# Optimization experiments

Hardware: AMD Instinct MI355X
Metric: run time of the kernel (lower is better)

## Reference

```python
import jax, jax.numpy as jnp
import numpy as np

ROPE_BASE = 10000.0

def _rms_norm(x):
    eps = jnp.asarray(jnp.finfo(x.dtype).eps, x.dtype)
    return x * jax.lax.rsqrt(jnp.mean(x * x, axis=-1, keepdims=True) + eps)

def _rope(x):
    # x: [B, S, H, hd]; rotate-halves variant: y1 = x1*cos + x2*sin, y2 = -x1*sin + x2*cos
    S, hd = x.shape[1], x.shape[3]
    d = hd // 2
    inv_freq = 1.0 / (ROPE_BASE ** (jnp.arange(0, hd, 2, dtype=jnp.float32) / hd))  # [d]
    t = jnp.arange(S, dtype=jnp.float32)
    freqs = jnp.outer(t, inv_freq)                       # [S, d]
    cos = jnp.cos(freqs)[None, :, None, :].astype(x.dtype)
    sin = jnp.sin(freqs)[None, :, None, :].astype(x.dtype)
    x1, x2 = x[..., :d], x[..., d:]
    return jnp.concatenate([x1 * cos + x2 * sin, -x1 * sin + x2 * cos], axis=-1)

def setup_inputs() -> dict:
    key = jax.random.key(0)
    ks = jax.random.split(key, 7)
    B, S, D = 1, 2048, 1024
    std = 0.02
    return {
        "x": jax.random.normal(ks[0], (B, S, D), jnp.float32),
        "v1": jax.random.normal(ks[1], (B, S, D), jnp.float32),
        "Wq": jax.random.normal(ks[2], (D, D), jnp.float32) * std,
        "Wk": jax.random.normal(ks[3], (D, D), jnp.float32) * std,
        "Wv": jax.random.normal(ks[4], (D, D), jnp.float32) * std,
        "Wout": jax.random.normal(ks[5], (D, D), jnp.float32) * std,
        "lambdas": jnp.float32(0.5),
        "n_heads": 16,
    }

def reference(x, v1, Wq, Wk, Wv, Wout, lambdas, n_heads):
    B, S, D = x.shape
    H = n_heads
    hd = D // H
    # QKV projections (CastedLinear, no bias)
    q = (x @ Wq.T).reshape(B, S, H, hd)
    k = (x @ Wk.T).reshape(B, S, H, hd)
    v = (x @ Wv.T).reshape(B, S, H, hd)
    # value residual mix with first-layer values v1
    v = (1.0 - lambdas) * v + lambdas * v1.reshape(B, S, H, hd)
    # per-head RMS norm (no learned scale) then RoPE
    q, k = _rms_norm(q), _rms_norm(k)
    q, k = _rope(q), _rope(k)
    # causal attention (flex_attention default: softmax, scale 1/sqrt(hd))
    scale = 1.0 / jnp.sqrt(jnp.asarray(hd, x.dtype))
    scores = jnp.einsum('bqhd,bkhd->bhqk', q, k) * scale        # [B,H,S,S]
    causal = jnp.tril(jnp.ones((S, S), dtype=bool))
    scores = jnp.where(causal[None, None], scores, jnp.asarray(-jnp.inf, scores.dtype))
    p = jax.nn.softmax(scores, axis=-1)
    y = jnp.einsum('bhqk,bkhd->bqhd', p, v).reshape(B, S, D)
    y = y @ Wout.T
    return (y, v1)
```

## Files before the change

### kernel.cpp

```cpp
#include <hip/hip_runtime.h>
#include <hip/hip_bf16.h>

#define S_LEN 2048
#define D_DIM 1024
#define NH    16
#define NEG_BIG (-1.0e30f)

#define EPI_NORMROPE   1
#define EPI_VMIX_T     2
#define EPI_F32        3
#define EPI_NORMROPE_Q 4

typedef __attribute__((ext_vector_type(8))) short bf16x8;
typedef __attribute__((ext_vector_type(4))) float f32x4;
typedef const __attribute__((address_space(1))) unsigned char gu8_t;
typedef __attribute__((address_space(3))) unsigned char lu8_t;

__device__ __forceinline__ float bf2f(unsigned short h) {
    union { unsigned int u; float f; } v; v.u = ((unsigned int)h) << 16; return v.f;
}
__device__ __forceinline__ unsigned short f2b(float f) {
    union { float f; unsigned int u; } v; v.f = f;
    unsigned int u = v.u;
    return (unsigned short)((u + 0x7FFFu + ((u >> 16) & 1u)) >> 16);
}
__device__ __forceinline__ unsigned short f2b_trunc(float f) {
    union { float f; unsigned int u; } v; v.f = f;
    return (unsigned short)(v.u >> 16);
}

__global__ __launch_bounds__(256)
void to_bf16(const float* __restrict__ x,  const float* __restrict__ wq,
             const float* __restrict__ wk, const float* __restrict__ wv,
             const float* __restrict__ wo, const float* __restrict__ v1,
             unsigned short* __restrict__ xb,  unsigned short* __restrict__ wqb,
             unsigned short* __restrict__ wkb, unsigned short* __restrict__ wvb,
             unsigned short* __restrict__ wob, float* __restrict__ v1dst)
{
    const int z = blockIdx.y;
    int i8 = blockIdx.x * 256 + threadIdx.x;
    if (z == 5) {
        const float* sp = v1 + (size_t)i8 * 8;
        float4 lo = *(const float4*)sp, hi = *(const float4*)(sp + 4);
        float* dp = v1dst + (size_t)i8 * 8;
        *(float4*)dp = lo; *(float4*)(dp + 4) = hi;
        return;
    }
    const float* s; unsigned short* d; int n;
    switch (z) {
        case 0: s = x;  d = xb;  n = S_LEN * D_DIM; break;
        case 1: s = wq; d = wqb; n = D_DIM * D_DIM; break;
        case 2: s = wk; d = wkb; n = D_DIM * D_DIM; break;
        case 3: s = wv; d = wvb; n = D_DIM * D_DIM; break;
        default: s = wo; d = wob; n = D_DIM * D_DIM; break;
    }
    if (i8 * 8 >= n) return;
    const float* sp = s + (size_t)i8 * 8;
    float4 lo = *(const float4*)sp, hi = *(const float4*)(sp + 4);
    uint4 p;
    p.x = f2b(lo.x) | ((unsigned)f2b(lo.y) << 16);
    p.y = f2b(lo.z) | ((unsigned)f2b(lo.w) << 16);
    p.z = f2b(hi.x) | ((unsigned)f2b(hi.y) << 16);
    p.w = f2b(hi.z) | ((unsigned)f2b(hi.w) << 16);
    *(uint4*)(d + (size_t)i8 * 8) = p;
}

__global__ __launch_bounds__(256, 3)
void gemm64(const unsigned short* __restrict__ A,
            const unsigned short* __restrict__ B0, const unsigned short* __restrict__ B1,
            const unsigned short* __restrict__ B2,
            void* __restrict__ C0, void* __restrict__ C1, void* __restrict__ C2,
            const float* __restrict__ vmix, const float* __restrict__ lam,
            int epiPack)
{
    const int which = blockIdx.z;
    const unsigned short* Bp = (which == 0) ? B0 : ((which == 1) ? B1 : B2);
    void* C = (which == 0) ? C0 : ((which == 1) ? C1 : C2);
    const int epi = (epiPack >> (8 * which)) & 0xff;
    const int tn = blockIdx.x * 128;
    const int tm = blockIdx.y * 64;

    __shared__ unsigned short Asl[64 * 32];
    __shared__ unsigned short Bsl[128 * 32];

    const int t    = threadIdx.x;
    const int lane = t & 63;
    const int wave = t >> 6;
    const int wm   = (wave >> 1) * 32;
    const int wn   = (wave & 1) * 64;
    const int lrow = lane & 15;
    const int quad = lane >> 4;
    const int srow = t >> 2;
    const int scol = (t & 3) * 8;

    f32x4 acc[2][4];
    #pragma unroll
    for (int i = 0; i < 2; ++i)
        #pragma unroll
        for (int j = 0; j < 4; ++j) {
            f32x4 z = {0.f, 0.f, 0.f, 0.f};
            acc[i][j] = z;
        }

    for (int k0 = 0; k0 < D_DIM; k0 += 32) {
        __builtin_amdgcn_global_load_lds(
            (gu8_t*)(A + (size_t)(tm + srow) * D_DIM + k0 + scol),
            (lu8_t*)&Asl[t * 8], 16, 0, 0);
        __builtin_amdgcn_global_load_lds(
            (gu8_t*)(Bp + (size_t)(tn + srow) * D_DIM + k0 + scol),
            (lu8_t*)&Bsl[t * 8], 16, 0, 0);
        __builtin_amdgcn_global_load_lds(
            (gu8_t*)(Bp + (size_t)(tn + 64 + srow) * D_DIM + k0 + scol),
            (lu8_t*)&Bsl[2048 + t * 8], 16, 0, 0);
        __syncthreads();
        bf16x8 af[2], bfr[4];
        #pragma unroll
        for (int i = 0; i < 2; ++i)
            af[i] = *(const bf16x8*)(&Asl[(wm + i * 16 + lrow) * 32 + quad * 8]);
        #pragma unroll
        for (int j = 0; j < 4; ++j)
            bfr[j] = *(const bf16x8*)(&Bsl[(wn + j * 16 + lrow) * 32 + quad * 8]);
        #pragma unroll
        for (int i = 0; i < 2; ++i)
            #pragma unroll
            for (int j = 0; j < 4; ++j)
                acc[i][j] = __builtin_amdgcn_mfma_f32_16x16x32_bf16(af[i], bfr[j], acc[i][j], 0, 0, 0);
        __syncthreads();
    }

    if (epi == EPI_NORMROPE || epi == EPI_NORMROPE_Q) {
        const float post = (epi == EPI_NORMROPE_Q) ? 0.18033688011112042f : 1.0f;
        #pragma unroll
        for (int i = 0; i < 2; ++i) {
            #pragma unroll
            for (int r = 0; r < 4; ++r) {
                int row = tm + wm + i * 16 + quad * 4 + r;
                float v0 = acc[i][0][r], v1 = acc[i][1][r];
                float v2 = acc[i][2][r], v3 = acc[i][3][r];
                float ss = v0 * v0 + v1 * v1 + v2 * v2 + v3 * v3;
                ss += __shfl_xor(ss, 1); ss += __shfl_xor(ss, 2);
                ss += __shfl_xor(ss, 4); ss += __shfl_xor(ss, 8);
                float rms = rsqrtf(ss * (1.f / 64.f) + 1.1920929e-7f) * post;
                v0 *= rms; v1 *= rms; v2 *= rms; v3 *= rms;
                float fs = (float)row;
                float a0 = fs * exp2f(-0.41524101186092030f * (float)lrow);
                float a1 = fs * exp2f(-0.41524101186092030f * (float)(16 + lrow));
                float s0, c0, s1, c1;
                __sincosf(a0, &s0, &c0);
                __sincosf(a1, &s1, &c1);
                unsigned short* Cb = (unsigned short*)C;
                size_t base = (size_t)row * D_DIM + tn + wn + lrow;
                Cb[base]      = f2b(v0 * c0 + v2 * s0);
                Cb[base + 16] = f2b(v1 * c1 + v3 * s1);
                Cb[base + 32] = f2b(-v0 * s0 + v2 * c0);
                Cb[base + 48] = f2b(-v1 * s1 + v3 * c1);
            }
        }
    } else if (epi == EPI_VMIX_T) {
        float lamf = *lam;
        #pragma unroll
        for (int i = 0; i < 2; ++i) {
            int cm0 = tm + wm + i * 16 + quad * 4;
            #pragma unroll
            for (int j = 0; j < 4; ++j) {
                int cn = tn + wn + j * 16 + lrow;
                ushort4 pk;
                float vals[4];
                #pragma unroll
                for (int r = 0; r < 4; ++r) {
                    size_t idx = (size_t)(cm0 + r) * D_DIM + cn;
                    vals[r] = (1.f - lamf) * acc[i][j][r] + lamf * vmix[idx];
                }
                pk.x = f2b(vals[0]); pk.y = f2b(vals[1]);
                pk.z = f2b(vals[2]); pk.w = f2b(vals[3]);
                *(ushort4*)((unsigned short*)C + (size_t)cn * S_LEN + cm0) = pk;
            }
        }
    } else {
        #pragma unroll
        for (int i = 0; i < 2; ++i) {
            int cm0 = tm + wm + i * 16 + quad * 4;
            #pragma unroll
            for (int j = 0; j < 4; ++j) {
                int cn = tn + wn + j * 16 + lrow;
                #pragma unroll
                for (int r = 0; r < 4; ++r)
                    ((float*)C)[(size_t)(cm0 + r) * D_DIM + cn] = acc[i][j][r];
            }
        }
    }
}

__global__ __launch_bounds__(256, 4)
void attn_mfma(const unsigned short* Qb,
               const unsigned short* __restrict__ Kb,
               const unsigned short* __restrict__ Vtg,
               float* __restrict__ Opart, float* __restrict__ Lpart)
{
    const int bx = blockIdx.x;
    int qb = 0, c = 0;
    {
        int accum = 0;
        #pragma unroll
        for (int q = 15; q >= 0; --q) {
            int n = (2 * q + 9) >> 3;
            if (bx >= accum && bx < accum + n) { qb = q; c = bx - accum; }
            accum += n;
        }
    }
    const int jmax = 2 * qb + 1;
    const int jlo  = c * 8;
    const int jhi  = min(jlo + 7, jmax);
    const int h  = blockIdx.y;
    const int t  = threadIdx.x;
    const int w  = t >> 6;
    const int l  = t & 63;
    const int l15  = l & 15;
    const int quad = l >> 4;
    const int hco  = h * 64;
    const int slot = (qb * 4 + c) * NH + h;

    __shared__ unsigned short Ks[2][64][72];
    __shared__ unsigned short Vt[2][64][72];

    bf16x8 qf[2][2];
    #pragma unroll
    for (int g = 0; g < 2; ++g) {
        const unsigned short* qrow =
            Qb + (size_t)(qb * 128 + w * 32 + g * 16 + l15) * D_DIM + hco;
        qf[g][0] = *(const bf16x8*)(qrow + quad * 8);
        qf[g][1] = *(const bf16x8*)(qrow + 32 + quad * 8);
    }

    f32x4 oac[2][4];
    #pragma unroll
    for (int g = 0; g < 2; ++g)
        #pragma unroll
        for (int nt = 0; nt < 4; ++nt) { f32x4 z = {0.f,0.f,0.f,0.f}; oac[g][nt] = z; }
    float lsum0 = 0.f, lsum1 = 0.f;

    const int rr = t >> 2;
    const int dc = (t & 3) * 16;

    const unsigned short* kbase = Kb  + (size_t)rr * D_DIM + hco + dc;
    const unsigned short* vbase = Vtg + (size_t)(hco + rr) * S_LEN + dc;

    uint4 ka0, ka1, va0, va1;
    {
        const unsigned short* kp = kbase + (size_t)jlo * 64 * D_DIM;
        const unsigned short* vp = vbase + (size_t)jlo * 64;
        ka0 = *(const uint4*)kp;  ka1 = *(const uint4*)(kp + 8);
        va0 = *(const uint4*)vp;  va1 = *(const uint4*)(vp + 8);
    }

    const float C2 = -11.541560327111707f;

    for (int j = jlo; j <= jhi; ++j) {
        const int buf = (j - jlo) & 1;
        *(uint4*)&Ks[buf][rr][dc]     = ka0;
        *(uint4*)&Ks[buf][rr][dc + 8] = ka1;
        *(uint4*)&Vt[buf][rr][dc]     = va0;
        *(uint4*)&Vt[buf][rr][dc + 8] = va1;
        __syncthreads();
        if (j < jhi) {
            const unsigned short* kp = kbase + (size_t)(j + 1) * 64 * D_DIM;
            const unsigned short* vp = vbase + (size_t)(j + 1) * 64;
            ka0 = *(const uint4*)kp;  ka1 = *(const uint4*)(kp + 8);
            va0 = *(const uint4*)vp;  va1 = *(const uint4*)(vp + 8);
        }

        unsigned short (*stale)[72] = (w < 2)
            ? (unsigned short (*)[72])&Ks[buf ^ 1][w * 32]
            : (unsigned short (*)[72])&Vt[buf ^ 1][(w - 2) * 32];
        const bool bulk = (j < 2 * qb);

        #pragma unroll
        for (int g = 0; g < 2; ++g) {
            f32x4 sac[4];
            __builtin_amdgcn_s_setprio(1);
            #pragma unroll
            for (int nt = 0; nt < 4; ++nt) {
                f32x4 z = {0.f,0.f,0.f,0.f};
                bf16x8 kf0 = *(const bf16x8*)&Ks[buf][nt * 16 + l15][quad * 8];
                z = __builtin_amdgcn_mfma_f32_16x16x32_bf16(kf0, qf[g][0], z, 0, 0, 0);
                bf16x8 kf1 = *(const bf16x8*)&Ks[buf][nt * 16 + l15][32 + quad * 8];
                z = __builtin_amdgcn_mfma_f32_16x16x32_bf16(kf1, qf[g][1], z, 0, 0, 0);
                sac[nt] = z;
            }
            __builtin_amdgcn_s_setprio(0);

            unsigned short (*Psw)[72] = (unsigned short (*)[72])&stale[g * 16];
            float lg = 0.f;
            if (bulk) {
                #pragma unroll
                for (int nt = 0; nt < 4; ++nt) {
                    float pe0 = exp2f(sac[nt][0] + C2);
                    float pe1 = exp2f(sac[nt][1] + C2);
                    float pe2 = exp2f(sac[nt][2] + C2);
                    float pe3 = exp2f(sac[nt][3] + C2);
                    lg += (pe0 + pe1) + (pe2 + pe3);
                    ushort4 pk;
                    pk.x = f2b_trunc(pe0); pk.y = f2b_trunc(pe1);
                    pk.z = f2b_trunc(pe2); pk.w = f2b_trunc(pe3);
                    *(ushort4*)&Psw[l15][nt * 16 + quad * 4] = pk;
                }
            } else {
                const int q_g = qb * 128 + w * 32 + g * 16 + l15;
                #pragma unroll
                for (int nt = 0; nt < 4; ++nt) {
                    int key0 = j * 64 + nt * 16 + quad * 4;
                    float pe[4];
                    #pragma unroll
                    for (int r = 0; r < 4; ++r) {
                        float s = sac[nt][r] + C2;
                        if (key0 + r > q_g) s = NEG_BIG;
                        pe[r] = exp2f(s);
                        lg += pe[r];
                    }
                    ushort4 pk;
                    pk.x = f2b_trunc(pe[0]); pk.y = f2b_trunc(pe[1]);
                    pk.z = f2b_trunc(pe[2]); pk.w = f2b_trunc(pe[3]);
                    *(ushort4*)&Psw[l15][nt * 16 + quad * 4] = pk;
                }
            }
            if (g == 0) lsum0 += lg; else lsum1 += lg;

            bf16x8 pf0 = *(const bf16x8*)&Psw[l15][quad * 8];
            bf16x8 pf1 = *(const bf16x8*)&Psw[l15][32 + quad * 8];
            __builtin_amdgcn_s_setprio(1);
            #pragma unroll
            for (int nt = 0; nt < 4; ++nt) {
                bf16x8 vf0 = *(const bf16x8*)&Vt[buf][nt * 16 + l15][quad * 8];
                oac[g][nt] = __builtin_amdgcn_mfma_f32_16x16x32_bf16(pf0, vf0, oac[g][nt], 0, 0, 0);
                bf16x8 vf1 = *(const bf16x8*)&Vt[buf][nt * 16 + l15][32 + quad * 8];
                oac[g][nt] = __builtin_amdgcn_mfma_f32_16x16x32_bf16(pf1, vf1, oac[g][nt], 0, 0, 0);
            }
            __builtin_amdgcn_s_setprio(0);
        }
        __syncthreads();
    }

    #pragma unroll
    for (int g = 0; g < 2; ++g) {
        float lr = (g == 0) ? lsum0 : lsum1;
        lr += __shfl_xor(lr, 16);
        lr += __shfl_xor(lr, 32);
        if (l < 16)
            Lpart[(size_t)slot * 128 + w * 32 + g * 16 + l15] = lr;
    }
    float* Op = Opart + (size_t)slot * 8192;
    #pragma unroll
    for (int g = 0; g < 2; ++g)
        #pragma unroll
        for (int nt = 0; nt < 4; ++nt)
            #pragma unroll
            for (int r = 0; r < 4; ++r)
                Op[(size_t)(w * 32 + g * 16 + quad * 4 + r) * 64 + nt * 16 + l15] = oac[g][nt][r];
}

__global__ __launch_bounds__(256)
void attn_combine(const float* __restrict__ Opart, const float* __restrict__ Lpart,
                  unsigned short* __restrict__ Ob)
{
    const int qb  = blockIdx.x;
    const int h   = blockIdx.y;
    const int t   = threadIdx.x;
    const int row = t >> 1;
    const int c0  = (t & 1) * 32;
    const int nchunks = (2 * qb + 9) >> 3;
    float acc[32];
    #pragma unroll
    for (int i = 0; i < 32; ++i) acc[i] = 0.f;
    float lsum = 0.f;
    for (int c = 0; c < nchunks; ++c) {
        const size_t slot = (size_t)((qb * 4 + c) * NH + h);
        const float* Op = Opart + slot * 8192 + (size_t)row * 64 + c0;
        #pragma unroll
        for (int g = 0; g < 8; ++g) {
            float4 a = *(const float4*)(Op + g * 4);
            acc[g * 4 + 0] += a.x; acc[g * 4 + 1] += a.y;
            acc[g * 4 + 2] += a.z; acc[g * 4 + 3] += a.w;
        }
        lsum += Lpart[slot * 128 + row];
    }
    const float inv = 1.f / lsum;
    unsigned int pk[16];
    #pragma unroll
    for (int i = 0; i < 16; ++i)
        pk[i] = f2b(acc[2 * i] * inv) | ((unsigned)f2b(acc[2 * i + 1] * inv) << 16);
    unsigned short* dst = Ob + (size_t)(qb * 128 + row) * D_DIM + h * 64 + c0;
    *(uint4*)dst        = make_uint4(pk[0],  pk[1],  pk[2],  pk[3]);
    *(uint4*)(dst + 8)  = make_uint4(pk[4],  pk[5],  pk[6],  pk[7]);
    *(uint4*)(dst + 16) = make_uint4(pk[8],  pk[9],  pk[10], pk[11]);
    *(uint4*)(dst + 24) = make_uint4(pk[12], pk[13], pk[14], pk[15]);
}

extern "C" void kernel_launch(void* const* d_in, const int* in_sizes, int n_in,
                              void* d_out, int out_size, void* d_ws, size_t ws_size,
                              hipStream_t stream)
{
    const float* x    = (const float*)d_in[0];
    const float* v1   = (const float*)d_in[1];
    const float* Wq   = (const float*)d_in[2];
    const float* Wk   = (const float*)d_in[3];
    const float* Wv   = (const float*)d_in[4];
    const float* Wout = (const float*)d_in[5];
    const float* lam  = (const float*)d_in[6];
    float* out = (float*)d_out;

    const size_t SD = (size_t)S_LEN * D_DIM;
    const size_t DD = (size_t)D_DIM * D_DIM;
    unsigned short* Qb  = (unsigned short*)d_ws;
    unsigned short* Kb  = Qb + SD;
    unsigned short* Vtg = Kb + SD;
    unsigned short* Ab  = Qb;
    float* Opart = (float*)(Vtg + SD);
    float* Lpart = Opart + (size_t)1024 * 8192;
    unsigned short* xb    = (unsigned short*)((char*)d_ws + (46u << 20));
    unsigned short* Woutb = (unsigned short*)((char*)d_ws + (50u << 20));

    unsigned short* Wqb   = (unsigned short*)d_out;
    unsigned short* Wkb   = Wqb + DD;
    unsigned short* Wvb   = Wkb + DD;

    to_bf16<<<dim3(1024, 6), 256, 0, stream>>>(
        x, Wq, Wk, Wv, Wout, v1, xb, Wqb, Wkb, Wvb, Woutb, out + SD);

    gemm64<<<dim3(D_DIM / 128, S_LEN / 64, 3), 256, 0, stream>>>(
        xb, Wqb, Wkb, Wvb, Qb, Kb, Vtg, v1, lam,
        EPI_NORMROPE_Q | (EPI_NORMROPE << 8) | (EPI_VMIX_T << 16));

    attn_mfma<<<dim3(40, NH), 256, 0, stream>>>(Qb, Kb, Vtg, Opart, Lpart);
    attn_combine<<<dim3(S_LEN / 128, NH), 256, 0, stream>>>(Opart, Lpart, Ab);

    gemm64<<<dim3(D_DIM / 128, S_LEN / 64, 1), 256, 0, stream>>>(
        Ab, Woutb, Woutb, Woutb, d_out, d_out, d_out, nullptr, lam, EPI_F32);
}
```

Measured before the change: 170.3 us.

## Restructure attention inner loop to share K/V fragments and add dedicated 64x64 output GEMM

Each attention tile iteration now loads every K fragment once and reuses it for both 16-row query groups. The probabilities are packed two bf16 values per word and written to LDS together before one combined PV phase, which reuses each V fragment across both groups. The output projection moves to a new 64x64-tile GEMM with twice as many blocks, meant to improve occupancy for the 1024-wide output. Register pressure in the attention kernel rises because all packed probabilities are held at once.

```diff
diff --git a/kernel.cpp b/kernel.cpp
--- a/kernel.cpp
+++ b/kernel.cpp
@@ -24,9 +24,9 @@
     unsigned int u = v.u;
     return (unsigned short)((u + 0x7FFFu + ((u >> 16) & 1u)) >> 16);
 }
-__device__ __forceinline__ unsigned short f2b_trunc(float f) {
-    union { float f; unsigned int u; } v; v.f = f;
-    return (unsigned short)(v.u >> 16);
+__device__ __forceinline__ unsigned int pack2(float a, float b) {
+    union { float f; unsigned int u; } x, y; x.f = a; y.f = b;
+    return (x.u >> 16) | (y.u & 0xFFFF0000u);
 }
 
 __global__ __launch_bounds__(256)
@@ -192,6 +192,72 @@
 }
 
 __global__ __launch_bounds__(256, 4)
+void gemm_out(const unsigned short* __restrict__ A,
+              const unsigned short* __restrict__ B,
+              float* __restrict__ C)
+{
+    const int tn = blockIdx.x * 64;
+    const int tm = blockIdx.y * 64;
+
+    __shared__ unsigned short Asl[64 * 32];
+    __shared__ unsigned short Bsl[64 * 32];
+
+    const int t    = threadIdx.x;
+    const int lane = t & 63;
+    const int wave = t >> 6;
+    const int wm   = (wave >> 1) * 32;
+    const int wn   = (wave & 1) * 32;
+    const int lrow = lane & 15;
+    const int quad = lane >> 4;
+    const int srow = t >> 2;
+    const int scol = (t & 3) * 8;
+
+    f32x4 acc[2][2];
+    #pragma unroll
+    for (int i = 0; i < 2; ++i)
+        #pragma unroll
+        for (int j = 0; j < 2; ++j) {
+            f32x4 z = {0.f, 0.f, 0.f, 0.f};
+            acc[i][j] = z;
+        }
+
+    for (int k0 = 0; k0 < D_DIM; k0 += 32) {
+        __builtin_amdgcn_global_load_lds(
+            (gu8_t*)(A + (size_t)(tm + srow) * D_DIM + k0 + scol),
+            (lu8_t*)&Asl[t * 8], 16, 0, 0);
+        __builtin_amdgcn_global_load_lds(
+            (gu8_t*)(B + (size_t)(tn + srow) * D_DIM + k0 + scol),
+            (lu8_t*)&Bsl[t * 8], 16, 0, 0);
+        __syncthreads();
+        bf16x8 af[2], bfr[2];
+        #pragma unroll
+        for (int i = 0; i < 2; ++i)
+            af[i] = *(const bf16x8*)(&Asl[(wm + i * 16 + lrow) * 32 + quad * 8]);
+        #pragma unroll
+        for (int j = 0; j < 2; ++j)
+            bfr[j] = *(const bf16x8*)(&Bsl[(wn + j * 16 + lrow) * 32 + quad * 8]);
+        #pragma unroll
+        for (int i = 0; i < 2; ++i)
+            #pragma unroll
+            for (int j = 0; j < 2; ++j)
+                acc[i][j] = __builtin_amdgcn_mfma_f32_16x16x32_bf16(af[i], bfr[j], acc[i][j], 0, 0, 0);
+        __syncthreads();
+    }
+
+    #pragma unroll
+    for (int i = 0; i < 2; ++i) {
+        int cm0 = tm + wm + i * 16 + quad * 4;
+        #pragma unroll
+        for (int j = 0; j < 2; ++j) {
+            int cn = tn + wn + j * 16 + lrow;
+            #pragma unroll
+            for (int r = 0; r < 4; ++r)
+                C[(size_t)(cm0 + r) * D_DIM + cn] = acc[i][j][r];
+        }
+    }
+}
+
+__global__ __launch_bounds__(256, 4)
 void attn_mfma(const unsigned short* Qb,
                const unsigned short* __restrict__ Kb,
                const unsigned short* __restrict__ Vtg,
@@ -274,69 +340,67 @@
             : (unsigned short (*)[72])&Vt[buf ^ 1][(w - 2) * 32];
         const bool bulk = (j < 2 * qb);
 
-        #pragma unroll
-        for (int g = 0; g < 2; ++g) {
-            f32x4 sac[4];
-            __builtin_amdgcn_s_setprio(1);
-            #pragma unroll
-            for (int nt = 0; nt < 4; ++nt) {
+        unsigned pw[2][4][2];
+        float ls0 = 0.f, ls1 = 0.f;
+        __builtin_amdgcn_s_setprio(1);
+        #pragma unroll
+        for (int nt = 0; nt < 4; ++nt) {
+            bf16x8 kf0 = *(const bf16x8*)&Ks[buf][nt * 16 + l15][quad * 8];
+            bf16x8 kf1 = *(const bf16x8*)&Ks[buf][nt * 16 + l15][32 + quad * 8];
+            #pragma unroll
+            for (int g = 0; g < 2; ++g) {
                 f32x4 z = {0.f,0.f,0.f,0.f};
-                bf16x8 kf0 = *(const bf16x8*)&Ks[buf][nt * 16 + l15][quad * 8];
                 z = __builtin_amdgcn_mfma_f32_16x16x32_bf16(kf0, qf[g][0], z, 0, 0, 0);
-                bf16x8 kf1 = *(const bf16x8*)&Ks[buf][nt * 16 + l15][32 + quad * 8];
                 z = __builtin_amdgcn_mfma_f32_16x16x32_bf16(kf1, qf[g][1], z, 0, 0, 0);
-                sac[nt] = z;
-            }
-            __builtin_amdgcn_s_setprio(0);
-
-            unsigned short (*Psw)[72] = (unsigned short (*)[72])&stale[g * 16];
-            float lg = 0.f;
-            if (bulk) {
-                #pragma unroll
-                for (int nt = 0; nt < 4; ++nt) {
-                    float pe0 = exp2f(sac[nt][0] + C2);
-                    float pe1 = exp2f(sac[nt][1] + C2);
-                    float pe2 = exp2f(sac[nt][2] + C2);
-                    float pe3 = exp2f(sac[nt][3] + C2);
-                    lg += (pe0 + pe1) + (pe2 + pe3);
-                    ushort4 pk;
-                    pk.x = f2b_trunc(pe0); pk.y = f2b_trunc(pe1);
-                    pk.z = f2b_trunc(pe2); pk.w = f2b_trunc(pe3);
-                    *(ushort4*)&Psw[l15][nt * 16 + quad * 4] = pk;
-                }
-            } else {
-                const int q_g = qb * 128 + w * 32 + g * 16 + l15;
-                #pragma unroll
-                for (int nt = 0; nt < 4; ++nt) {
-                    int key0 = j * 64 + nt * 16 + quad * 4;
-                    float pe[4];
+                float pe[4];
+                if (bulk) {
+                    #pragma unroll
+                    for (int r = 0; r < 4; ++r) pe[r] = exp2f(z[r] + C2);
+                } else {
+                    const int q_g  = qb * 128 + w * 32 + g * 16 + l15;
+                    const int key0 = j * 64 + nt * 16 + quad * 4;
                     #pragma unroll
                     for (int r = 0; r < 4; ++r) {
-                        float s = sac[nt][r] + C2;
+                        float s = z[r] + C2;
                         if (key0 + r > q_g) s = NEG_BIG;
                         pe[r] = exp2f(s);
-                        lg += pe[r];
                     }
-                    ushort4 pk;
-                    pk.x = f2b_trunc(pe[0]); pk.y = f2b_trunc(pe[1]);
-                    pk.z = f2b_trunc(pe[2]); pk.w = f2b_trunc(pe[3]);
-                    *(ushort4*)&Psw[l15][nt * 16 + quad * 4] = pk;
                 }
+                float psum = (pe[0] + pe[1]) + (pe[2] + pe[3]);
+                if (g == 0) ls0 += psum; else ls1 += psum;
+                pw[g][nt][0] = pack2(pe[0], pe[1]);
+                pw[g][nt][1] = pack2(pe[2], pe[3]);
             }
-            if (g == 0) lsum0 += lg; else lsum1 += lg;
-
-            bf16x8 pf0 = *(const bf16x8*)&Psw[l15][quad * 8];
-            bf16x8 pf1 = *(const bf16x8*)&Psw[l15][32 + quad * 8];
-            __builtin_amdgcn_s_setprio(1);
+        }
+        __builtin_amdgcn_s_setprio(0);
+        lsum0 += ls0; lsum1 += ls1;
+
+        #pragma unroll
+        for (int g = 0; g < 2; ++g)
             #pragma unroll
             for (int nt = 0; nt < 4; ++nt) {
-                bf16x8 vf0 = *(const bf16x8*)&Vt[buf][nt * 16 + l15][quad * 8];
-                oac[g][nt] = __builtin_amdgcn_mfma_f32_16x16x32_bf16(pf0, vf0, oac[g][nt], 0, 0, 0);
-                bf16x8 vf1 = *(const bf16x8*)&Vt[buf][nt * 16 + l15][32 + quad * 8];
-                oac[g][nt] = __builtin_amdgcn_mfma_f32_16x16x32_bf16(pf1, vf1, oac[g][nt], 0, 0, 0);
+                uint2 pk; pk.x = pw[g][nt][0]; pk.y = pw[g][nt][1];
+                *(uint2*)&stale[g * 16 + l15][nt * 16 + quad * 4] = pk;
             }
-            __builtin_amdgcn_s_setprio(0);
-        }
+
+        bf16x8 pf[2][2];
+        #pragma unroll
+        for (int g = 0; g < 2; ++g) {
+            pf[g][0] = *(const bf16x8*)&stale[g * 16 + l15][quad * 8];
+            pf[g][1] = *(const bf16x8*)&stale[g * 16 + l15][32 + quad * 8];
+        }
+
+        __builtin_amdgcn_s_setprio(1);
+        #pragma unroll
+        for (int nt = 0; nt < 4; ++nt) {
+            bf16x8 vf0 = *(const bf16x8*)&Vt[buf][nt * 16 + l15][quad * 8];
+            bf16x8 vf1 = *(const bf16x8*)&Vt[buf][nt * 16 + l15][32 + quad * 8];
+            oac[0][nt] = __builtin_amdgcn_mfma_f32_16x16x32_bf16(pf[0][0], vf0, oac[0][nt], 0, 0, 0);
+            oac[0][nt] = __builtin_amdgcn_mfma_f32_16x16x32_bf16(pf[0][1], vf1, oac[0][nt], 0, 0, 0);
+            oac[1][nt] = __builtin_amdgcn_mfma_f32_16x16x32_bf16(pf[1][0], vf0, oac[1][nt], 0, 0, 0);
+            oac[1][nt] = __builtin_amdgcn_mfma_f32_16x16x32_bf16(pf[1][1], vf1, oac[1][nt], 0, 0, 0);
+        }
+        __builtin_amdgcn_s_setprio(0);
         __syncthreads();
     }
 
@@ -433,6 +497,5 @@
     attn_mfma<<<dim3(40, NH), 256, 0, stream>>>(Qb, Kb, Vtg, Opart, Lpart);
     attn_combine<<<dim3(S_LEN / 128, NH), 256, 0, stream>>>(Opart, Lpart, Ab);
 
-    gemm64<<<dim3(D_DIM / 128, S_LEN / 64, 1), 256, 0, stream>>>(
-        Ab, Woutb, Woutb, Woutb, d_out, d_out, d_out, nullptr, lam, EPI_F32);
-}
+    gemm_out<<<dim3(D_DIM / 64, S_LEN / 64), 256, 0, stream>>>(Ab, Woutb, out);
+}
```

Result: faster. 166.9 us (-2.0%).
